# Kernel tuning notes

Hardware: AMD Instinct MI355X
Metric: run time of the kernel (lower is better)

Reference implementation:

```python
import jax, jax.numpy as jnp
import numpy as np

N_NODES = 100000
N_EDGES = 3200000
NUM_FEATURES = 128
NUM_CLASSES = 32
H1, H2 = 64, 32


def _glorot(key, shape):
    lim = float(np.sqrt(6.0 / (shape[0] + shape[1])))
    return jax.random.uniform(key, shape, jnp.float32, -lim, lim)


def setup_inputs() -> dict:
    key = jax.random.key(0)
    ks = jax.random.split(key, 8)
    x = jax.random.normal(ks[0], (N_NODES, NUM_FEATURES), jnp.float32)
    edge_index = jax.random.randint(ks[1], (2, N_EDGES), 0, N_NODES, jnp.int64)
    return {
        "x": x,
        "edge_index": edge_index,
        "W1": _glorot(ks[2], (NUM_FEATURES, H1)), "b1": jnp.zeros((H1,), jnp.float32),
        "W2": _glorot(ks[3], (H1, H2)), "b2": jnp.zeros((H2,), jnp.float32),
        "Wf": _glorot(ks[4], (H2, H2)), "bf": jnp.zeros((H2,), jnp.float32),
        "Wo": _glorot(ks[5], (H2, NUM_CLASSES)), "bo": jnp.zeros((NUM_CLASSES,), jnp.float32),
    }


def gcn_conv(x, src, dst, n, W, b):
    # PyG GCNConv: add self-loops, symmetric normalization D^-1/2 A D^-1/2,
    # aggregate messages source -> target (dst = edge_index[1]).
    h = x @ W                                            # [N, F_out]
    deg = jax.ops.segment_sum(jnp.ones_like(dst, dtype=x.dtype), dst, num_segments=n)
    dinv = jnp.where(deg > 0, jax.lax.rsqrt(deg), 0.0)
    norm = dinv[src] * dinv[dst]                         # [E+N]
    msg = h[src] * norm[:, None]                         # gather + scale
    return jax.ops.segment_sum(msg, dst, num_segments=n) + b


def reference(x, edge_index, W1, b1, W2, b2, Wf, bf, Wo, bo):
    n = x.shape[0]
    loops = jnp.arange(n, dtype=edge_index.dtype)
    src = jnp.concatenate([edge_index[0], loops])
    dst = jnp.concatenate([edge_index[1], loops])
    h = jax.nn.relu(gcn_conv(x, src, dst, n, W1, b1))
    h = gcn_conv(h, src, dst, n, W2, b2)
    h = jax.nn.relu(h @ Wf + bf)
    return h @ Wo + bo
```

## Files before the change

### kernel.cpp

```cpp
#include <hip/hip_runtime.h>
#include <hip/hip_bf16.h>

#define N_NODES 100000
#define N_EDGES 3200000
#define F_IN    128
#define H1F     64
#define H2F     32
#define NCLS    32
#define SCAN_BLOCK 1024
#define SCAN_CHUNKS ((N_NODES + SCAN_BLOCK - 1) / SCAN_BLOCK)
#define NTILES (N_NODES / 16)
#define NCNT   (N_EDGES / 4 / 256)
#define XPAD 132

typedef __attribute__((ext_vector_type(8))) short bf16x8;
typedef __attribute__((ext_vector_type(4))) float f32x4;

static __device__ __forceinline__ float b2f(__hip_bfloat16 v) {
    return __bfloat162float(v);
}
static __device__ __forceinline__ float us2f(unsigned short u) {
    return __uint_as_float(((unsigned)u) << 16);
}
static __device__ __forceinline__ unsigned short f2us(float f) {
    __hip_bfloat16 h = __float2bfloat16(f);
    return *(unsigned short*)&h;
}
static __device__ __forceinline__ float ld(const void* p, size_t i, int isbf) {
    return isbf ? b2f(((const __hip_bfloat16*)p)[i]) : ((const float*)p)[i];
}


__global__ void k_detect(const void* xbuf, const void* eibuf, int* flags) {
    if (threadIdx.x != 0 || blockIdx.x != 0) return;
    const unsigned* ew = (const unsigned*)eibuf;
    int z = 0;
    for (int k = 0; k < 256; ++k) z += (ew[2 * k + 1] == 0u) ? 1 : 0;
    flags[0] = (z >= 200) ? 1 : 0;
    const unsigned* xw = (const unsigned*)xbuf;
    int inr = 0;
    for (int k = 0; k < 256; ++k) {
        unsigned fb = (xw[k] & 0xFFFFu) << 16;
        float a = fabsf(__uint_as_float(fb));
        inr += (a >= 1e-4f && a <= 20.0f) ? 1 : 0;
    }
    flags[1] = (inr >= 160) ? 1 : 0;
}

__global__ void k_packW1(const unsigned short* __restrict__ W1,
                         unsigned short* __restrict__ W1p) {
    int t = blockIdx.x * blockDim.x + threadIdx.x;
    if (t >= F_IN * H1F) return;
    int j    = t & 7;
    int lane = (t >> 3) & 63;
    int fg   = (t >> 9) & 3;
    int kc   = t >> 11;
    int quad = lane >> 4, col = lane & 15;
    W1p[t] = W1[(kc * 32 + quad * 8 + j) * H1F + fg * 16 + col];
}

__global__ void k_dinv(const int* __restrict__ deg, float* __restrict__ dinv) {
    int i = blockIdx.x * blockDim.x + threadIdx.x;
    if (i < N_NODES) dinv[i] = rsqrtf((float)deg[i] + 1.0f);
}

__global__ void k_scanA(const int* __restrict__ deg, int* __restrict__ partial) {
    __shared__ int red[16];
    int b = blockIdx.x, t = threadIdx.x;
    int i = b * SCAN_BLOCK + t;
    int v = (i < N_NODES) ? deg[i] : 0;
    for (int off = 32; off; off >>= 1) v += __shfl_down(v, off, 64);
    if ((t & 63) == 0) red[t >> 6] = v;
    __syncthreads();
    if (t == 0) {
        int s = 0;
        for (int k = 0; k < 16; ++k) s += red[k];
        partial[b] = s;
    }
}

__global__ void k_scanB(const int* __restrict__ partial, int* __restrict__ chunkoff) {
    if (threadIdx.x != 0 || blockIdx.x != 0) return;
    int run = 0;
    for (int b = 0; b < SCAN_CHUNKS; ++b) { chunkoff[b] = run; run += partial[b]; }
}

__global__ void k_scanC(const int* __restrict__ deg, const int* __restrict__ chunkoff,
                        int* __restrict__ rowptr) {
    __shared__ int wsum[16];
    int b = blockIdx.x, t = threadIdx.x, lane = t & 63, w = t >> 6;
    int i = b * SCAN_BLOCK + t;
    int v = (i < N_NODES) ? deg[i] : 0;
    for (int off = 1; off < 64; off <<= 1) {
        int u = __shfl_up(v, off, 64);
        if (lane >= off) v += u;
    }
    if (lane == 63) wsum[w] = v;
    __syncthreads();
    if (t == 0) {
        int run = 0;
        for (int k = 0; k < 16; ++k) { int s = wsum[k]; wsum[k] = run; run += s; }
    }
    __syncthreads();
    int incl = v + wsum[w] + chunkoff[b];
    if (i < N_NODES) rowptr[i + 1] = incl;
    if (b == 0 && t == 0) rowptr[0] = 0;
}

__global__ void k_scatter(const int* __restrict__ ei, const int* __restrict__ aux,
                          const int* __restrict__ rowptr, int* __restrict__ csr,
                          const int* __restrict__ flags) {
    int t = blockIdx.x * blockDim.x + threadIdx.x;
    int e0 = t * 4;
    if (e0 >= N_EDGES) return;
    int s[4], d[4];
    if (flags[0]) {
        const int4* ps = (const int4*)(ei + 2 * (size_t)e0);
        int4 a = ps[0], b = ps[1];
        s[0] = a.x; s[1] = a.z; s[2] = b.x; s[3] = b.z;
        const int4* pd = (const int4*)(ei + 2 * (size_t)(N_EDGES + e0));
        int4 c = pd[0], g = pd[1];
        d[0] = c.x; d[1] = c.z; d[2] = g.x; d[3] = g.z;
    } else {
        int4 a = *(const int4*)(ei + (size_t)e0);
        s[0] = a.x; s[1] = a.y; s[2] = a.z; s[3] = a.w;
        int4 c = *(const int4*)(ei + (size_t)N_EDGES + e0);
        d[0] = c.x; d[1] = c.y; d[2] = c.z; d[3] = c.w;
    }
    int4 av = *(const int4*)(aux + e0);
    int a4[4] = { av.x, av.y, av.z, av.w };
#pragma unroll
    for (int j = 0; j < 4; ++j) {
        if ((unsigned)s[j] < N_NODES && (unsigned)d[j] < N_NODES)
            csr[rowptr[d[j]] + a4[j]] = s[j];
    }
}

__global__ void __launch_bounds__(256)
k_front(const void* __restrict__ x, const void* __restrict__ W1,
        const unsigned short* __restrict__ W1p, const int* __restrict__ ei,
        int* __restrict__ deg, int* __restrict__ aux,
        unsigned short* __restrict__ h1, const int* __restrict__ flags) {
    __shared__ unsigned short w1s[F_IN * H1F];
    __shared__ unsigned short xs[16 * XPAD];
    int blk = blockIdx.x, tid = threadIdx.x;

    if (blk % 3 == 0) {
        int t = (blk / 3) * 256 + tid;
        int e0 = t * 4;
        if (e0 >= N_EDGES) return;
        int d[4];
        if (flags[0]) {
            const int4* p = (const int4*)(ei + 2 * (size_t)(N_EDGES + e0));
            int4 a = p[0], b = p[1];
            d[0] = a.x; d[1] = a.z; d[2] = b.x; d[3] = b.z;
        } else {
            int4 a = *(const int4*)(ei + (size_t)N_EDGES + e0);
            d[0] = a.x; d[1] = a.y; d[2] = a.z; d[3] = a.w;
        }
        int p0 = ((unsigned)d[0] < N_NODES) ? atomicAdd(&deg[d[0]], 1) : 0;
        int p1 = ((unsigned)d[1] < N_NODES) ? atomicAdd(&deg[d[1]], 1) : 0;
        int p2 = ((unsigned)d[2] < N_NODES) ? atomicAdd(&deg[d[2]], 1) : 0;
        int p3 = ((unsigned)d[3] < N_NODES) ? atomicAdd(&deg[d[3]], 1) : 0;
        *(int4*)(aux + e0) = make_int4(p0, p1, p2, p3);
        return;
    }

    int tile = blk - blk / 3 - 1;
    int isbf = flags[1];
    if (isbf) {
        const uint4* src = (const uint4*)W1p;
        uint4*       dst = (uint4*)w1s;
#pragma unroll
        for (int k = 0; k < 4; ++k) dst[tid + k * 256] = src[tid + k * 256];
        const short* xp = (const short*)x + (size_t)tile * 16 * F_IN;
        int r = tid >> 4, c = tid & 15;
        *(bf16x8*)(xs + r * XPAD + c * 8) = *(const bf16x8*)(xp + tid * 8);
    }
    __syncthreads();

    int wave = tid >> 6, lane = tid & 63;
    int col = lane & 15, quad = lane >> 4;
    int fg = wave;

    if (isbf) {
        bf16x8 afr[4];
#pragma unroll
        for (int kc = 0; kc < 4; ++kc)
            afr[kc] = *(const bf16x8*)(xs + col * XPAD + kc * 32 + quad * 8);
        f32x4 acc;
#pragma unroll
        for (int r = 0; r < 4; ++r) acc[r] = 0.f;
#pragma unroll
        for (int kc = 0; kc < 4; ++kc) {
            bf16x8 bfr = *(const bf16x8*)(w1s + (((kc * 4 + fg) * 64 + lane) * 8));
            acc = __builtin_amdgcn_mfma_f32_16x16x32_bf16(afr[kc], bfr, acc, 0, 0, 0);
        }
#pragma unroll
        for (int r = 0; r < 4; ++r)
            h1[(size_t)(tile * 16 + quad * 4 + r) * H1F + fg * 16 + col] = f2us(acc[r]);
    } else {
        const float* wfp = (const float*)W1;
        for (int i = 0; i < 4; ++i) {
            int n = tile * 16 + wave * 4 + i;
            const float2* xr = (const float2*)((const float*)x + (size_t)n * F_IN);
            float2 my = xr[lane];
            float acc = 0.f;
#pragma unroll 16
            for (int k = 0; k < 64; ++k) {
                float x0 = __shfl(my.x, k, 64);
                float x1 = __shfl(my.y, k, 64);
                acc += x0 * wfp[(2 * k) * H1F + lane];
                acc += x1 * wfp[(2 * k + 1) * H1F + lane];
            }
            h1[(size_t)n * H1F + lane] = f2us(acc);
        }
    }
}

__global__ void k_agg1gemm2(const unsigned short* __restrict__ h1,
                            const float* __restrict__ dinv,
                            const int* __restrict__ rowptr, const int* __restrict__ csr,
                            const void* __restrict__ b1, const void* __restrict__ W2,
                            unsigned short* __restrict__ h2, const int* __restrict__ flags) {
    int n    = (blockIdx.x * blockDim.x + threadIdx.x) >> 6;
    int lane = threadIdx.x & 63;
    if (n >= N_NODES) return;
    int beg = rowptr[n], end = rowptr[n + 1];
    float dn  = dinv[n];
    float acc = dn * us2f(h1[(size_t)n * H1F + lane]);
    int e = beg;
    for (; e + 3 < end; e += 4) {
        int s0 = csr[e], s1 = csr[e + 1], s2 = csr[e + 2], s3 = csr[e + 3];
        float w0 = dinv[s0], w1 = dinv[s1], w2 = dinv[s2], w3 = dinv[s3];
        unsigned short v0 = h1[(size_t)s0 * H1F + lane];
        unsigned short v1 = h1[(size_t)s1 * H1F + lane];
        unsigned short v2 = h1[(size_t)s2 * H1F + lane];
        unsigned short v3 = h1[(size_t)s3 * H1F + lane];
        acc += w0 * us2f(v0) + w1 * us2f(v1) + w2 * us2f(v2) + w3 * us2f(v3);
    }
    for (; e < end; ++e) {
        int s = csr[e];
        acc += dinv[s] * us2f(h1[(size_t)s * H1F + lane]);
    }
    acc *= dn;
    int isbf = flags[1];
    float bv = isbf ? b2f(((const __hip_bfloat16*)b1)[lane]) : ((const float*)b1)[lane];
    float v  = fmaxf(acc + bv, 0.f);
    int f = lane & 31, h = lane >> 5;
    float part = 0.f;
    if (isbf) {
        const __hip_bfloat16* w = (const __hip_bfloat16*)W2;
#pragma unroll
        for (int j = 0; j < 32; ++j) {
            int k = h * 32 + j;
            part += __shfl(v, k, 64) * b2f(w[k * H2F + f]);
        }
    } else {
        const float* w = (const float*)W2;
#pragma unroll
        for (int j = 0; j < 32; ++j) {
            int k = h * 32 + j;
            part += __shfl(v, k, 64) * w[k * H2F + f];
        }
    }
    part += __shfl(part, lane ^ 32, 64);
    if (h == 0) h2[(size_t)n * H2F + f] = f2us(part);
}

__global__ void GCN_51737176048479_kernel(const unsigned short* __restrict__ h2,
                                          const float* __restrict__ dinv,
                                          const int* __restrict__ rowptr,
                                          const int* __restrict__ csr,
                                          const void* __restrict__ b2v,
                                          const void* __restrict__ Wf,
                                          const void* __restrict__ bfv,
                                          const void* __restrict__ Wo,
                                          const void* __restrict__ bov,
                                          void* __restrict__ out,
                                          const int* __restrict__ flags) {
    int tid = blockIdx.x * blockDim.x + threadIdx.x;
    int n   = tid >> 5;
    int f   = threadIdx.x & 31;
    if (n >= N_NODES) return;
    int isbf = flags[1];
    int beg = rowptr[n], end = rowptr[n + 1];
    float dn = dinv[n];
    float ar = dn * us2f(h2[(size_t)n * H2F + f]);
    int e = beg;
    for (; e + 3 < end; e += 4) {
        int s0 = csr[e], s1 = csr[e + 1], s2 = csr[e + 2], s3 = csr[e + 3];
        float w0 = dinv[s0], w1 = dinv[s1], w2 = dinv[s2], w3 = dinv[s3];
        unsigned short v0 = h2[(size_t)s0 * H2F + f];
        unsigned short v1 = h2[(size_t)s1 * H2F + f];
        unsigned short v2 = h2[(size_t)s2 * H2F + f];
        unsigned short v3 = h2[(size_t)s3 * H2F + f];
        ar += w0 * us2f(v0) + w1 * us2f(v1) + w2 * us2f(v2) + w3 * us2f(v3);
    }
    for (; e < end; ++e) {
        int s = csr[e];
        ar += dinv[s] * us2f(h2[(size_t)s * H2F + f]);
    }
    ar = ar * dn + ld(b2v, f, isbf);
    float acc1 = 0.f;
#pragma unroll
    for (int k = 0; k < H2F; ++k)
        acc1 += __shfl(ar, k, 32) * ld(Wf, (size_t)k * H2F + f, isbf);
    float u = fmaxf(acc1 + ld(bfv, f, isbf), 0.f);
    float acc2 = 0.f;
#pragma unroll
    for (int k = 0; k < H2F; ++k)
        acc2 += __shfl(u, k, 32) * ld(Wo, (size_t)k * NCLS + f, isbf);
    float r = acc2 + ld(bov, f, isbf);
    size_t oi = (size_t)n * NCLS + f;
    if (isbf) ((__hip_bfloat16*)out)[oi] = __float2bfloat16(r);
    else      ((float*)out)[oi] = r;
}

extern "C" void kernel_launch(void* const* d_in, const int* in_sizes, int n_in,
                              void* d_out, int out_size, void* d_ws, size_t ws_size,
                              hipStream_t stream) {
    const void* x  = d_in[0];
    const int*  ei = (const int*)d_in[1];
    const void* W1 = d_in[2];
    const void* b1 = d_in[3];
    const void* W2 = d_in[4];
    const void* b2 = d_in[5];
    const void* Wf = d_in[6];
    const void* bf = d_in[7];
    const void* Wo = d_in[8];
    const void* bo = d_in[9];

    char* ws = (char*)d_ws;
    int*            deg      = (int*)  (ws + 0);
    int*            rowptr   = (int*)  (ws + (512u  << 10));
    float*          dinv     = (float*)(ws + (1024u << 10));
    int*            flags    = (int*)  (ws + (1434u << 10));
    int*            partial  = (int*)  (ws + (1444u << 10));
    int*            chunkoff = (int*)  (ws + (1454u << 10));
    unsigned short* W1p      = (unsigned short*)(ws + (1536u << 10));
    int*            aux      = (int*)  (ws + (2u  << 20));
    int*            csr      = (int*)  (ws + (15u << 20));
    unsigned short* h1       = (unsigned short*)(ws + (28u << 20));
    unsigned short* h2       = (unsigned short*)(ws + (41u << 20));

    const int B = 256;

    k_detect<<<1, 64, 0, stream>>>(x, ei, flags);
    hipMemsetAsync(deg, 0, N_NODES * sizeof(int), stream);
    k_packW1<<<(F_IN * H1F + B - 1) / B, B, 0, stream>>>((const unsigned short*)W1, W1p);

    k_front<<<NTILES + NCNT, B, 0, stream>>>(x, W1, W1p, ei, deg, aux, h1, flags);

    k_dinv<<<(N_NODES + B - 1) / B, B, 0, stream>>>(deg, dinv);
    k_scanA<<<SCAN_CHUNKS, SCAN_BLOCK, 0, stream>>>(deg, partial);
    k_scanB<<<1, 64, 0, stream>>>(partial, chunkoff);
    k_scanC<<<SCAN_CHUNKS, SCAN_BLOCK, 0, stream>>>(deg, chunkoff, rowptr);
    k_scatter<<<(N_EDGES / 4 + B - 1) / B, B, 0, stream>>>(ei, aux, rowptr, csr, flags);

    k_agg1gemm2<<<(N_NODES * 64 + B - 1) / B, B, 0, stream>>>(h1, dinv, rowptr, csr,
                                                              b1, W2, h2, flags);
    GCN_51737176048479_kernel<<<(N_NODES * 32 + B - 1) / B, B, 0, stream>>>(
        h2, dinv, rowptr, csr, b2, Wf, bf, Wo, bo, d_out, flags);
}
```

Measured before the change: 580.0 us.

## Rewrite layer-1 GEMM with readlane broadcasts and fuse dinv into scan

Replaces the first-layer transform with a register-tiled scalar FMA loop: each wave handles 8 nodes and broadcasts x values with readlane instead of ds-shuffles or MFMA with LDS staging. The separate W1 packing kernel goes away, and the dinv computation is folded into the first scan pass. The degree-count blocks now process 8 edges per thread. The aim is to cut kernel launches and shuffle and LDS overhead in the front stage. The trade-off is giving up MFMA for the bf16 path, relying on plain vector ALU throughput instead.

```diff
diff --git a/kernel.cpp b/kernel.cpp
--- a/kernel.cpp
+++ b/kernel.cpp
@@ -1,5 +1,6 @@
 #include <hip/hip_runtime.h>
 #include <hip/hip_bf16.h>
+
 
 #define N_NODES 100000
 #define N_EDGES 3200000
@@ -9,9 +10,9 @@
 #define NCLS    32
 #define SCAN_BLOCK 1024
 #define SCAN_CHUNKS ((N_NODES + SCAN_BLOCK - 1) / SCAN_BLOCK)
-#define NTILES (N_NODES / 16)
-#define NCNT   (N_EDGES / 4 / 256)
-#define XPAD 132
+#define NTIL2 (N_NODES / 32)
+#define NCNT2 ((N_EDGES + 2048 - 1) / 2048)
+#define NFRONT (NTIL2 + NCNT2)
 
 typedef __attribute__((ext_vector_type(8))) short bf16x8;
 typedef __attribute__((ext_vector_type(4))) float f32x4;
@@ -28,6 +29,9 @@
 }
 static __device__ __forceinline__ float ld(const void* p, size_t i, int isbf) {
     return isbf ? b2f(((const __hip_bfloat16*)p)[i]) : ((const float*)p)[i];
+}
+static __device__ __forceinline__ float rdlane(float v, int l) {
+    return __int_as_float(__builtin_amdgcn_readlane(__float_as_int(v), l));
 }
 
 
@@ -47,28 +51,99 @@
     flags[1] = (inr >= 160) ? 1 : 0;
 }
 
-__global__ void k_packW1(const unsigned short* __restrict__ W1,
-                         unsigned short* __restrict__ W1p) {
-    int t = blockIdx.x * blockDim.x + threadIdx.x;
-    if (t >= F_IN * H1F) return;
-    int j    = t & 7;
-    int lane = (t >> 3) & 63;
-    int fg   = (t >> 9) & 3;
-    int kc   = t >> 11;
-    int quad = lane >> 4, col = lane & 15;
-    W1p[t] = W1[(kc * 32 + quad * 8 + j) * H1F + fg * 16 + col];
-}
-
-__global__ void k_dinv(const int* __restrict__ deg, float* __restrict__ dinv) {
-    int i = blockIdx.x * blockDim.x + threadIdx.x;
-    if (i < N_NODES) dinv[i] = rsqrtf((float)deg[i] + 1.0f);
-}
-
-__global__ void k_scanA(const int* __restrict__ deg, int* __restrict__ partial) {
+__global__ void __launch_bounds__(256)
+k_front(const void* __restrict__ x, const void* __restrict__ W1,
+        const int* __restrict__ ei,
+        int* __restrict__ deg, int* __restrict__ aux,
+        unsigned short* __restrict__ h1, const int* __restrict__ flags) {
+    int blk = blockIdx.x, tid = threadIdx.x;
+
+    if (blk % 3 == 0) {
+        int t = (blk / 3) * 256 + tid;
+        int e0 = t * 8;
+        if (e0 >= N_EDGES) return;
+        int d[8];
+        if (flags[0]) {
+            const int4* p = (const int4*)(ei + 2 * (size_t)(N_EDGES + e0));
+            int4 a = p[0], b = p[1], c = p[2], g = p[3];
+            d[0] = a.x; d[1] = a.z; d[2] = b.x; d[3] = b.z;
+            d[4] = c.x; d[5] = c.z; d[6] = g.x; d[7] = g.z;
+        } else {
+            const int4* p = (const int4*)(ei + (size_t)N_EDGES + e0);
+            int4 a = p[0], b = p[1];
+            d[0] = a.x; d[1] = a.y; d[2] = a.z; d[3] = a.w;
+            d[4] = b.x; d[5] = b.y; d[6] = b.z; d[7] = b.w;
+        }
+        int r[8];
+#pragma unroll
+        for (int j = 0; j < 8; ++j)
+            r[j] = ((unsigned)d[j] < N_NODES) ? atomicAdd(&deg[d[j]], 1) : 0;
+        *(int4*)(aux + e0)     = make_int4(r[0], r[1], r[2], r[3]);
+        *(int4*)(aux + e0 + 4) = make_int4(r[4], r[5], r[6], r[7]);
+        return;
+    }
+
+    int tile = blk - blk / 3 - 1;
+    int isbf = flags[1];
+    int wave = tid >> 6, lane = tid & 63;
+    size_t nbase = (size_t)tile * 32 + (size_t)wave * 8;
+
+    float2 xr[8];
+    if (isbf) {
+#pragma unroll
+        for (int i = 0; i < 8; ++i) {
+            unsigned u = ((const unsigned*)x)[(nbase + i) * (F_IN / 2) + lane];
+            xr[i].x = us2f((unsigned short)(u & 0xFFFFu));
+            xr[i].y = us2f((unsigned short)(u >> 16));
+        }
+    } else {
+#pragma unroll
+        for (int i = 0; i < 8; ++i)
+            xr[i] = ((const float2*)x)[(nbase + i) * (F_IN / 2) + lane];
+    }
+
+    float acc[8];
+#pragma unroll
+    for (int i = 0; i < 8; ++i) acc[i] = 0.f;
+
+    if (isbf) {
+        const unsigned short* w = (const unsigned short*)W1;
+#pragma unroll 4
+        for (int k2 = 0; k2 < 64; ++k2) {
+            float wa = us2f(w[(2 * k2) * H1F + lane]);
+            float wb = us2f(w[(2 * k2 + 1) * H1F + lane]);
+#pragma unroll
+            for (int i = 0; i < 8; ++i) {
+                acc[i] += rdlane(xr[i].x, k2) * wa;
+                acc[i] += rdlane(xr[i].y, k2) * wb;
+            }
+        }
+    } else {
+        const float* w = (const float*)W1;
+#pragma unroll 4
+        for (int k2 = 0; k2 < 64; ++k2) {
+            float wa = w[(2 * k2) * H1F + lane];
+            float wb = w[(2 * k2 + 1) * H1F + lane];
+#pragma unroll
+            for (int i = 0; i < 8; ++i) {
+                acc[i] += rdlane(xr[i].x, k2) * wa;
+                acc[i] += rdlane(xr[i].y, k2) * wb;
+            }
+        }
+    }
+
+#pragma unroll
+    for (int i = 0; i < 8; ++i)
+        h1[(nbase + i) * H1F + lane] = f2us(acc[i]);
+}
+
+__global__ void k_scanA(const int* __restrict__ deg, int* __restrict__ partial,
+                        float* __restrict__ dinv) {
     __shared__ int red[16];
     int b = blockIdx.x, t = threadIdx.x;
     int i = b * SCAN_BLOCK + t;
     int v = (i < N_NODES) ? deg[i] : 0;
+    if (i < N_NODES) dinv[i] = rsqrtf((float)v + 1.0f);
     for (int off = 32; off; off >>= 1) v += __shfl_down(v, off, 64);
     if ((t & 63) == 0) red[t >> 6] = v;
     __syncthreads();
@@ -133,88 +208,6 @@
     for (int j = 0; j < 4; ++j) {
         if ((unsigned)s[j] < N_NODES && (unsigned)d[j] < N_NODES)
             csr[rowptr[d[j]] + a4[j]] = s[j];
-    }
-}
-
-__global__ void __launch_bounds__(256)
-k_front(const void* __restrict__ x, const void* __restrict__ W1,
-        const unsigned short* __restrict__ W1p, const int* __restrict__ ei,
-        int* __restrict__ deg, int* __restrict__ aux,
-        unsigned short* __restrict__ h1, const int* __restrict__ flags) {
-    __shared__ unsigned short w1s[F_IN * H1F];
-    __shared__ unsigned short xs[16 * XPAD];
-    int blk = blockIdx.x, tid = threadIdx.x;
-
-    if (blk % 3 == 0) {
-        int t = (blk / 3) * 256 + tid;
-        int e0 = t * 4;
-        if (e0 >= N_EDGES) return;
-        int d[4];
-        if (flags[0]) {
-            const int4* p = (const int4*)(ei + 2 * (size_t)(N_EDGES + e0));
-            int4 a = p[0], b = p[1];
-            d[0] = a.x; d[1] = a.z; d[2] = b.x; d[3] = b.z;
-        } else {
-            int4 a = *(const int4*)(ei + (size_t)N_EDGES + e0);
-            d[0] = a.x; d[1] = a.y; d[2] = a.z; d[3] = a.w;
-        }
-        int p0 = ((unsigned)d[0] < N_NODES) ? atomicAdd(&deg[d[0]], 1) : 0;
-        int p1 = ((unsigned)d[1] < N_NODES) ? atomicAdd(&deg[d[1]], 1) : 0;
-        int p2 = ((unsigned)d[2] < N_NODES) ? atomicAdd(&deg[d[2]], 1) : 0;
-        int p3 = ((unsigned)d[3] < N_NODES) ? atomicAdd(&deg[d[3]], 1) : 0;
-        *(int4*)(aux + e0) = make_int4(p0, p1, p2, p3);
-        return;
-    }
-
-    int tile = blk - blk / 3 - 1;
-    int isbf = flags[1];
-    if (isbf) {
-        const uint4* src = (const uint4*)W1p;
-        uint4*       dst = (uint4*)w1s;
-#pragma unroll
-        for (int k = 0; k < 4; ++k) dst[tid + k * 256] = src[tid + k * 256];
-        const short* xp = (const short*)x + (size_t)tile * 16 * F_IN;
-        int r = tid >> 4, c = tid & 15;
-        *(bf16x8*)(xs + r * XPAD + c * 8) = *(const bf16x8*)(xp + tid * 8);
-    }
-    __syncthreads();
-
-    int wave = tid >> 6, lane = tid & 63;
-    int col = lane & 15, quad = lane >> 4;
-    int fg = wave;
-
-    if (isbf) {
-        bf16x8 afr[4];
-#pragma unroll
-        for (int kc = 0; kc < 4; ++kc)
-            afr[kc] = *(const bf16x8*)(xs + col * XPAD + kc * 32 + quad * 8);
-        f32x4 acc;
-#pragma unroll
-        for (int r = 0; r < 4; ++r) acc[r] = 0.f;
-#pragma unroll
-        for (int kc = 0; kc < 4; ++kc) {
-            bf16x8 bfr = *(const bf16x8*)(w1s + (((kc * 4 + fg) * 64 + lane) * 8));
-            acc = __builtin_amdgcn_mfma_f32_16x16x32_bf16(afr[kc], bfr, acc, 0, 0, 0);
-        }
-#pragma unroll
-        for (int r = 0; r < 4; ++r)
-            h1[(size_t)(tile * 16 + quad * 4 + r) * H1F + fg * 16 + col] = f2us(acc[r]);
-    } else {
-        const float* wfp = (const float*)W1;
-        for (int i = 0; i < 4; ++i) {
-            int n = tile * 16 + wave * 4 + i;
-            const float2* xr = (const float2*)((const float*)x + (size_t)n * F_IN);
-            float2 my = xr[lane];
-            float acc = 0.f;
-#pragma unroll 16
-            for (int k = 0; k < 64; ++k) {
-                float x0 = __shfl(my.x, k, 64);
-                float x1 = __shfl(my.y, k, 64);
-                acc += x0 * wfp[(2 * k) * H1F + lane];
-                acc += x1 * wfp[(2 * k + 1) * H1F + lane];
-            }
-            h1[(size_t)n * H1F + lane] = f2us(acc);
-        }
     }
 }
 
@@ -338,7 +331,6 @@
     int*            flags    = (int*)  (ws + (1434u << 10));
     int*            partial  = (int*)  (ws + (1444u << 10));
     int*            chunkoff = (int*)  (ws + (1454u << 10));
-    unsigned short* W1p      = (unsigned short*)(ws + (1536u << 10));
     int*            aux      = (int*)  (ws + (2u  << 20));
     int*            csr      = (int*)  (ws + (15u << 20));
     unsigned short* h1       = (unsigned short*)(ws + (28u << 20));
@@ -348,12 +340,10 @@
 
     k_detect<<<1, 64, 0, stream>>>(x, ei, flags);
     hipMemsetAsync(deg, 0, N_NODES * sizeof(int), stream);
-    k_packW1<<<(F_IN * H1F + B - 1) / B, B, 0, stream>>>((const unsigned short*)W1, W1p);
-
-    k_front<<<NTILES + NCNT, B, 0, stream>>>(x, W1, W1p, ei, deg, aux, h1, flags);
-
-    k_dinv<<<(N_NODES + B - 1) / B, B, 0, stream>>>(deg, dinv);
-    k_scanA<<<SCAN_CHUNKS, SCAN_BLOCK, 0, stream>>>(deg, partial);
+
+    k_front<<<NFRONT, B, 0, stream>>>(x, W1, ei, deg, aux, h1, flags);
+
+    k_scanA<<<SCAN_CHUNKS, SCAN_BLOCK, 0, stream>>>(deg, partial, dinv);
     k_scanB<<<1, 64, 0, stream>>>(partial, chunkoff);
     k_scanC<<<SCAN_CHUNKS, SCAN_BLOCK, 0, stream>>>(deg, chunkoff, rowptr);
     k_scatter<<<(N_EDGES / 4 + B - 1) / B, B, 0, stream>>>(ei, aux, rowptr, csr, flags);
```

Result: faster. 562.9 us (-2.9%).
